# Optimization experiments

Measured on AMD Instinct MI355X. Metric: run time of the kernel, lower is better.

The kernel has to match this reference:

```python
import jax, jax.numpy as jnp
import numpy as np

NODE_SIZE = 50000
REL_SIZE = 2000
TRIPLE_SIZE = 1000000
HID = 128
DEPTH = 2


def _rows_covering(key, n_rows, n_seg):
    # sorted row indices guaranteeing every segment appears at least once
    extra = jax.random.randint(key, (n_rows - n_seg,), 0, n_seg)
    return jnp.sort(jnp.concatenate([jnp.arange(n_seg), extra])).astype(jnp.int32)


def setup_inputs() -> dict:
    key = jax.random.key(0)
    ks = jax.random.split(key, 12)
    adj = jnp.stack([_rows_covering(ks[0], TRIPLE_SIZE, NODE_SIZE),
                     jax.random.randint(ks[1], (TRIPLE_SIZE,), 0, NODE_SIZE, dtype=jnp.int32)])
    r_index = jnp.stack([jnp.arange(TRIPLE_SIZE, dtype=jnp.int32),
                         jax.random.randint(ks[2], (TRIPLE_SIZE,), 0, REL_SIZE, dtype=jnp.int32)])
    r_val = jax.random.uniform(ks[3], (TRIPLE_SIZE,), dtype=jnp.float32)
    ent_adj = jnp.stack([_rows_covering(ks[4], TRIPLE_SIZE, NODE_SIZE),
                         jax.random.randint(ks[5], (TRIPLE_SIZE,), 0, NODE_SIZE, dtype=jnp.int32)])
    rel_adj = jnp.stack([_rows_covering(ks[6], TRIPLE_SIZE, NODE_SIZE),
                         jax.random.randint(ks[7], (TRIPLE_SIZE,), 0, REL_SIZE, dtype=jnp.int32)])
    ent_emb = jax.random.normal(ks[8], (NODE_SIZE, HID), dtype=jnp.float32) * 0.05
    rel_emb = jax.random.normal(ks[9], (REL_SIZE, HID), dtype=jnp.float32) * 0.05
    attn_e = jax.random.normal(ks[10], (DEPTH, HID, 1), dtype=jnp.float32) * 0.1
    attn_r = jax.random.normal(ks[11], (DEPTH, HID, 1), dtype=jnp.float32) * 0.1
    return {"ent_emb": ent_emb, "rel_emb": rel_emb, "attn_e": attn_e, "attn_r": attn_r,
            "adj": adj, "r_index": r_index, "r_val": r_val,
            "ent_adj": ent_adj, "rel_adj": rel_adj}


def _avg(adj, emb, node_size):
    # sparse softmax over all-ones values == mean over neighbors
    rows, cols = adj[0], adj[1]
    deg = jax.ops.segment_sum(jnp.ones_like(rows, dtype=emb.dtype), rows, node_size)
    s = jax.ops.segment_sum(emb[cols], rows, node_size)  # [node_size, d]
    return s / jnp.maximum(deg, 1.0)[:, None]


def _segment_softmax(vals, seg, num_seg):
    m = jax.ops.segment_max(vals, seg, num_seg)
    e = jnp.exp(vals - m[seg])
    s = jax.ops.segment_sum(e, seg, num_seg)
    return e / s[seg]


def _nr_graph_attention(features, rel_emb, adj, r_index, r_val, attn_kernels):
    feats = jnp.tanh(features)
    outs = [feats]
    src, dst = adj[0], adj[1]
    for l in range(DEPTH):
        # sparse [T, R] @ rel_emb -> per-triple relation vector
        tri_rel = jax.ops.segment_sum(r_val[:, None] * rel_emb[r_index[1]], r_index[0], TRIPLE_SIZE)
        tri_rel = tri_rel / jnp.maximum(jnp.linalg.norm(tri_rel, axis=1, keepdims=True), 1e-12)
        neighs = feats[dst]  # [T, H]
        # Householder reflection of neighbor feature about tri_rel
        neighs = neighs - 2.0 * jnp.sum(neighs * tri_rel, axis=1, keepdims=True) * tri_rel
        att = jnp.squeeze(tri_rel @ attn_kernels[l], axis=-1)  # [T]
        a = _segment_softmax(att, src, NODE_SIZE)
        feats = jnp.tanh(jax.ops.segment_sum(neighs * a[:, None], src, NODE_SIZE))
        outs.append(feats)
    return jnp.concatenate(outs, axis=-1)  # [N, H*(DEPTH+1)]


def reference(ent_emb, rel_emb, attn_e, attn_r, adj, r_index, r_val, ent_adj, rel_adj):
    ent_feature = _avg(ent_adj, ent_emb, NODE_SIZE)  # [N, H]
    rel_feature = _avg(rel_adj, rel_emb, NODE_SIZE)  # [N, H]
    out_rel = _nr_graph_attention(rel_feature, rel_emb, adj, r_index, r_val, attn_r)
    out_ent = _nr_graph_attention(ent_feature, rel_emb, adj, r_index, r_val, attn_e)
    return jnp.concatenate([out_ent, out_rel], axis=-1)  # dropout rate 0 -> identity
```

## Files before the change

kernel.cpp:

```cpp
#include <hip/hip_runtime.h>
#include <hip/hip_fp16.h>
#include <math.h>

#define NN 50000
#define NR 2000
#define NT 1000000
#define HID 128
#define OSTRIDE 768
#define CH 256

typedef float f32x4 __attribute__((ext_vector_type(4)));
typedef unsigned u32x4 __attribute__((ext_vector_type(4)));
typedef unsigned u32x2 __attribute__((ext_vector_type(2)));
typedef _Float16 h16x2 __attribute__((ext_vector_type(2)));
typedef _Float16 h16x8 __attribute__((ext_vector_type(8)));

union U4H8 { u32x4 u; h16x8 h; };

__device__ __forceinline__ float wsum64(float v) {
#pragma unroll
  for (int off = 32; off > 0; off >>= 1) v += __shfl_xor(v, off, 64);
  return v;
}
__device__ __forceinline__ unsigned pack2(float x, float y) {
  __half2 h = __floats2half2_rn(x, y);
  union { __half2 h; unsigned u; } c; c.h = h; return c.u;
}
__device__ __forceinline__ float2 unpack2(unsigned u) {
  union { unsigned u; __half2 h; } c; c.u = u;
  return __half22float2(c.h);
}
__device__ __forceinline__ void nt_store4(const float4& v, float* p) {
  f32x4 t = {v.x, v.y, v.z, v.w};
  __builtin_nontemporal_store(t, (f32x4*)p);
}

__global__ void rowptr3_kernel(const int* __restrict__ a0, int* __restrict__ r0,
                               const int* __restrict__ a1, int* __restrict__ r1,
                               const int* __restrict__ a2, int* __restrict__ r2) {
  const int* rows = (blockIdx.y == 0) ? a0 : (blockIdx.y == 1) ? a1 : a2;
  int* rp = (blockIdx.y == 0) ? r0 : (blockIdx.y == 1) ? r1 : r2;
  int i = blockIdx.x * blockDim.x + threadIdx.x;
  int stride = gridDim.x * blockDim.x;
  for (int t = i; t < NT; t += stride) {
    if (t == 0 || rows[t] != rows[t - 1]) rp[rows[t]] = t;
  }
  if (i == 0) rp[NN] = NT;
}

__global__ __launch_bounds__(256) void prep_kernel(
    const float* __restrict__ rel_emb, const float* __restrict__ attn_e,
    const float* __restrict__ attn_r, float4* __restrict__ e4,
    float* __restrict__ n2i_arr, const float* __restrict__ ent_emb,
    __half* __restrict__ enth, __half* __restrict__ relh) {
  int wid = (blockIdx.x * blockDim.x + threadIdx.x) >> 6;
  int lane = threadIdx.x & 63;
  if (wid < NR) {
    const float2* e2 = (const float2*)rel_emb;
    float2 e = e2[(size_t)wid * 64 + lane];
    float p = wsum64(e.x * e.x + e.y * e.y);
    float inv_n = rsqrtf(p);
    const float* ks[4] = {attn_e, attn_e + HID, attn_r, attn_r + HID};
    float d[4];
#pragma unroll
    for (int j = 0; j < 4; ++j) {
      float2 a = ((const float2*)ks[j])[lane];
      d[j] = wsum64(e.x * a.x + e.y * a.y);
    }
    if (lane == 0) {
      e4[wid] = make_float4(expf(d[0] * inv_n), expf(d[1] * inv_n),
                            expf(d[2] * inv_n), expf(d[3] * inv_n));
      n2i_arr[wid] = 1.f / p;
    }
    return;
  }
  int i = (wid - NR) * 64 + lane;
  const int entu = NN * 16;
  const float4* s4;
  u32x4* d;
  int j;
  if (i < entu) {
    s4 = (const float4*)ent_emb; d = (u32x4*)enth; j = i;
  } else {
    j = i - entu;
    if (j >= NR * 16) return;
    s4 = (const float4*)rel_emb; d = (u32x4*)relh;
  }
  float4 a = s4[2 * j], b = s4[2 * j + 1];
  u32x4 w;
  w.x = pack2(a.x, a.y); w.y = pack2(a.z, a.w);
  w.z = pack2(b.x, b.y); w.w = pack2(b.z, b.w);
  __builtin_nontemporal_store(w, d + j);
}

__global__ __launch_bounds__(256) void avgwpre_kernel(
    const int* __restrict__ rp_ent, const int* __restrict__ cols_ent,
    const int* __restrict__ rp_rel, const int* __restrict__ cols_rel,
    const __half* __restrict__ enth, const __half* __restrict__ relh,
    float* __restrict__ out, __half* __restrict__ c0h,
    const int* __restrict__ rp_adj, const int* __restrict__ dst,
    const int* __restrict__ rel_id, const float* __restrict__ r_val,
    const float4* __restrict__ e4, const float* __restrict__ n2i_arr,
    unsigned* __restrict__ pk, u32x2* __restrict__ wq0,
    u32x2* __restrict__ wq1) {
  int wid = (blockIdx.x * blockDim.x + threadIdx.x) >> 6;
  int lane = threadIdx.x & 63;

  if (wid < NN) {
    int br = (wid >= NN / 2) ? 1 : 0;
    int pair = wid - br * (NN / 2);
    int node = pair * 2 + (lane >> 5);
    int sl = lane & 31;
    const int* rp = br ? rp_rel : rp_ent;
    const int* cols = br ? cols_rel : cols_ent;
    const u32x2* eb = (const u32x2*)(br ? relh : enth);
    int t0 = rp[node], t1 = rp[node + 1];
    int nmax = t1 - 1;
    int i0 = cols[t0];
    int i1 = cols[min(t0 + 1, nmax)];
    int i2 = cols[min(t0 + 2, nmax)];
    int i3 = cols[min(t0 + 3, nmax)];
    int i4 = cols[min(t0 + 4, nmax)];
    int i5 = cols[min(t0 + 5, nmax)];
    int i6 = cols[min(t0 + 6, nmax)];
    int i7 = cols[min(t0 + 7, nmax)];
    float4 acc = make_float4(0.f, 0.f, 0.f, 0.f);
    const u32x2 z = {0u, 0u};
    for (int t = t0; t < t1; t += 8) {
      u32x2 h0 = eb[(size_t)i0 * 32 + sl];
      u32x2 h1 = eb[(size_t)i1 * 32 + sl];
      u32x2 h2 = eb[(size_t)i2 * 32 + sl];
      u32x2 h3 = eb[(size_t)i3 * 32 + sl];
      u32x2 h4 = eb[(size_t)i4 * 32 + sl];
      u32x2 h5 = eb[(size_t)i5 * 32 + sl];
      u32x2 h6 = eb[(size_t)i6 * 32 + sl];
      u32x2 h7 = eb[(size_t)i7 * 32 + sl];
      int tn = t + 8;
      i0 = cols[min(tn, nmax)];
      i1 = cols[min(tn + 1, nmax)];
      i2 = cols[min(tn + 2, nmax)];
      i3 = cols[min(tn + 3, nmax)];
      i4 = cols[min(tn + 4, nmax)];
      i5 = cols[min(tn + 5, nmax)];
      i6 = cols[min(tn + 6, nmax)];
      i7 = cols[min(tn + 7, nmax)];
      h1 = (t + 1 < t1) ? h1 : z;
      h2 = (t + 2 < t1) ? h2 : z;
      h3 = (t + 3 < t1) ? h3 : z;
      h4 = (t + 4 < t1) ? h4 : z;
      h5 = (t + 5 < t1) ? h5 : z;
      h6 = (t + 6 < t1) ? h6 : z;
      h7 = (t + 7 < t1) ? h7 : z;
      float2 a0 = unpack2(h0.x), b0 = unpack2(h0.y);
      float2 a1 = unpack2(h1.x), b1 = unpack2(h1.y);
      float2 a2 = unpack2(h2.x), b2 = unpack2(h2.y);
      float2 a3 = unpack2(h3.x), b3 = unpack2(h3.y);
      float2 a4 = unpack2(h4.x), b4 = unpack2(h4.y);
      float2 a5 = unpack2(h5.x), b5 = unpack2(h5.y);
      float2 a6 = unpack2(h6.x), b6 = unpack2(h6.y);
      float2 a7 = unpack2(h7.x), b7 = unpack2(h7.y);
      acc.x += ((a0.x + a1.x) + (a2.x + a3.x)) + ((a4.x + a5.x) + (a6.x + a7.x));
      acc.y += ((a0.y + a1.y) + (a2.y + a3.y)) + ((a4.y + a5.y) + (a6.y + a7.y));
      acc.z += ((b0.x + b1.x) + (b2.x + b3.x)) + ((b4.x + b5.x) + (b6.x + b7.x));
      acc.w += ((b0.y + b1.y) + (b2.y + b3.y)) + ((b4.y + b5.y) + (b6.y + b7.y));
    }
    float inv = 1.f / (float)(t1 - t0);
    float4 o;
    o.x = tanhf(acc.x * inv); o.y = tanhf(acc.y * inv);
    o.z = tanhf(acc.z * inv); o.w = tanhf(acc.w * inv);
    nt_store4(o, out + (size_t)node * OSTRIDE + (br ? 3 * HID : 0) + sl * 4);
    u32x2 w; w.x = pack2(o.x, o.y); w.y = pack2(o.z, o.w);
    __builtin_nontemporal_store(w,
        (u32x2*)(c0h + (size_t)node * CH + br * HID + sl * 4));
    return;
  }

  wid -= NN;
  if (wid >= NN / 4) return;
  int sub = lane >> 4;
  int s = lane & 15;
  int node = wid * 4 + sub;
  int t0 = rp_adj[node], t1 = rp_adj[node + 1];
  float4 ss = make_float4(0.f, 0.f, 0.f, 0.f);
  for (int t = t0 + s; t < t1; t += 16) {
    int r = rel_id[t];
    float rv = r_val[t];
    float4 ex = e4[r];
    if (rv <= 0.f) ex = make_float4(1.f, 1.f, 1.f, 1.f);
    ss.x += ex.x; ss.y += ex.y; ss.z += ex.z; ss.w += ex.w;
  }
#pragma unroll
  for (int off = 1; off < 16; off <<= 1) {
    ss.x += __shfl_xor(ss.x, off, 64);
    ss.y += __shfl_xor(ss.y, off, 64);
    ss.z += __shfl_xor(ss.z, off, 64);
    ss.w += __shfl_xor(ss.w, off, 64);
  }
  float4 inv = make_float4(1.f / ss.x, 1.f / ss.y, 1.f / ss.z, 1.f / ss.w);
  for (int t = t0 + s; t < t1; t += 16) {
    int r = rel_id[t];
    float rv = r_val[t];
    int dn = dst[t];
    float4 ex = e4[r];
    float zi = n2i_arr[r];
    if (rv <= 0.f) { ex = make_float4(1.f, 1.f, 1.f, 1.f); zi = 0.f; }
    float we0 = ex.x * inv.x, wr0 = ex.z * inv.z;
    float we1 = ex.y * inv.y, wr1 = ex.w * inv.w;
    __builtin_nontemporal_store((unsigned)dn | ((unsigned)r << 16), pk + t);
    u32x2 a, b;
    a.x = pack2(we0, wr0); a.y = pack2(-2.f * we0 * zi, -2.f * wr0 * zi);
    b.x = pack2(we1, wr1); b.y = pack2(-2.f * we1 * zi, -2.f * wr1 * zi);
    __builtin_nontemporal_store(a, wq0 + t);
    __builtin_nontemporal_store(b, wq1 + t);
  }
}

struct RecT { int dn; int r; float we, wr, ce, cr; };

__device__ __forceinline__ RecT ldrec(int t, int t1,
                                      const unsigned* __restrict__ pk,
                                      const u32x2* __restrict__ wq) {
  bool valid = (t < t1);
  int tc = valid ? t : (t1 - 1);
  unsigned p = pk[tc];
  u32x2 w = wq[tc];
  RecT rec;
  rec.dn = (int)(p & 0xFFFFu);
  rec.r = (int)(p >> 16);
  float2 a = unpack2(w.x);
  float2 b = unpack2(w.y);
  rec.we = valid ? a.x : 0.f;
  rec.wr = valid ? a.y : 0.f;
  rec.ce = valid ? b.x : 0.f;
  rec.cr = valid ? b.y : 0.f;
  return rec;
}

__global__ __launch_bounds__(256) void attn_kernel(
    float* __restrict__ out, const int* __restrict__ rp,
    const unsigned* __restrict__ pk, const u32x2* __restrict__ wq,
    const __half* __restrict__ relh, const __half* __restrict__ chin,
    __half* __restrict__ chout, int layer) {
  int wid = (blockIdx.x * blockDim.x + threadIdx.x) >> 6;
  int lane = threadIdx.x & 63;
  if (wid >= NN) return;
  int g = lane >> 4;
  int sl = lane & 15;
  int t0 = rp[wid], t1 = rp[wid + 1];

  const u32x4* relh4 = (const u32x4*)relh;
  RecT A = ldrec(t0 + g, t1, pk, wq);
  RecT B = ldrec(t0 + 4 + g, t1, pk, wq);
  float aE[8], aR[8];
#pragma unroll
  for (int i = 0; i < 8; ++i) { aE[i] = 0.f; aR[i] = 0.f; }

  for (int tb = t0; tb < t1; tb += 8) {
    U4H8 uhA, ehA, qhA, uhB, ehB, qhB;
    uhA.u = relh4[(size_t)A.r * 16 + sl];
    const u32x4* phA = (const u32x4*)chin + (size_t)A.dn * 32;
    ehA.u = phA[sl];
    qhA.u = phA[16 + sl];
    uhB.u = relh4[(size_t)B.r * 16 + sl];
    const u32x4* phB = (const u32x4*)chin + (size_t)B.dn * 32;
    ehB.u = phB[sl];
    qhB.u = phB[16 + sl];
    RecT An = ldrec(tb + 8 + g, t1, pk, wq);
    RecT Bn = ldrec(tb + 12 + g, t1, pk, wq);

    float deA = 0.f, drA = 0.f, deB = 0.f, drB = 0.f;
#if __has_builtin(__builtin_amdgcn_fdot2)
#pragma unroll
    for (int i = 0; i < 4; ++i) {
      h16x2 uA = {uhA.h[2 * i], uhA.h[2 * i + 1]};
      h16x2 eA = {ehA.h[2 * i], ehA.h[2 * i + 1]};
      h16x2 qA = {qhA.h[2 * i], qhA.h[2 * i + 1]};
      h16x2 uB = {uhB.h[2 * i], uhB.h[2 * i + 1]};
      h16x2 eB = {ehB.h[2 * i], ehB.h[2 * i + 1]};
      h16x2 qB = {qhB.h[2 * i], qhB.h[2 * i + 1]};
      deA = __builtin_amdgcn_fdot2(uA, eA, deA, false);
      drA = __builtin_amdgcn_fdot2(uA, qA, drA, false);
      deB = __builtin_amdgcn_fdot2(uB, eB, deB, false);
      drB = __builtin_amdgcn_fdot2(uB, qB, drB, false);
    }
#else
#pragma unroll
    for (int i = 0; i < 8; ++i) {
      deA += (float)uhA.h[i] * (float)ehA.h[i];
      drA += (float)uhA.h[i] * (float)qhA.h[i];
      deB += (float)uhB.h[i] * (float)ehB.h[i];
      drB += (float)uhB.h[i] * (float)qhB.h[i];
    }
#endif
#pragma unroll
    for (int off = 1; off < 16; off <<= 1) {
      deA += __shfl_xor(deA, off, 64);
      drA += __shfl_xor(drA, off, 64);
      deB += __shfl_xor(deB, off, 64);
      drB += __shfl_xor(drB, off, 64);
    }
    float ceA = A.ce * deA;
    float crA = A.cr * drA;
    float ceB = B.ce * deB;
    float crB = B.cr * drB;
#pragma unroll
    for (int i = 0; i < 8; ++i) {
      float ufA = (float)uhA.h[i];
      float ufB = (float)uhB.h[i];
      aE[i] += A.we * (float)ehA.h[i] + ceA * ufA;
      aE[i] += B.we * (float)ehB.h[i] + ceB * ufB;
      aR[i] += A.wr * (float)qhA.h[i] + crA * ufA;
      aR[i] += B.wr * (float)qhB.h[i] + crB * ufB;
    }
    A = An;
    B = Bn;
  }

#pragma unroll
  for (int i = 0; i < 8; ++i) {
    aE[i] += __shfl_xor(aE[i], 16, 64);
    aE[i] += __shfl_xor(aE[i], 32, 64);
    aR[i] += __shfl_xor(aR[i], 16, 64);
    aR[i] += __shfl_xor(aR[i], 32, 64);
  }

  float4 v;
  if (g == 0) v = make_float4(aE[0], aE[1], aE[2], aE[3]);
  else if (g == 1) v = make_float4(aE[4], aE[5], aE[6], aE[7]);
  else if (g == 2) v = make_float4(aR[0], aR[1], aR[2], aR[3]);
  else v = make_float4(aR[4], aR[5], aR[6], aR[7]);
  v.x = tanhf(v.x); v.y = tanhf(v.y); v.z = tanhf(v.z); v.w = tanhf(v.w);
  float* ob = (g < 2) ? (out + (size_t)wid * OSTRIDE + (layer + 1) * HID)
                      : (out + (size_t)wid * OSTRIDE + (4 + layer) * HID);
  nt_store4(v, ob + sl * 8 + (g & 1) * 4);
  if (chout) {
    u32x2 w; w.x = pack2(v.x, v.y); w.y = pack2(v.z, v.w);
    __builtin_nontemporal_store(
        w, (u32x2*)(chout + (size_t)wid * CH + (g >> 1) * 128 + sl * 8 + (g & 1) * 4));
  }
}

extern "C" void kernel_launch(void* const* d_in, const int* in_sizes, int n_in,
                              void* d_out, int out_size, void* d_ws, size_t ws_size,
                              hipStream_t stream) {
  const float* ent_emb = (const float*)d_in[0];
  const float* rel_emb = (const float*)d_in[1];
  const float* attn_e = (const float*)d_in[2];
  const float* attn_r = (const float*)d_in[3];
  const int* adj = (const int*)d_in[4];
  const int* r_index = (const int*)d_in[5];
  const float* r_val = (const float*)d_in[6];
  const int* ent_adj = (const int*)d_in[7];
  const int* rel_adj = (const int*)d_in[8];
  float* out = (float*)d_out;

  char* ws = (char*)d_ws;
  __half* enth = (__half*)ws;  ws += (size_t)NN * HID * sizeof(__half);
  __half* relh = (__half*)ws;  ws += (size_t)NR * HID * sizeof(__half);
  __half* C0h = (__half*)ws;   ws += (size_t)NN * CH * sizeof(__half);
  __half* C1h = (__half*)ws;   ws += (size_t)NN * CH * sizeof(__half);
  unsigned* pk = (unsigned*)ws; ws += (size_t)NT * sizeof(unsigned);
  u32x2* wq0 = (u32x2*)ws;     ws += (size_t)NT * sizeof(u32x2);
  u32x2* wq1 = (u32x2*)ws;     ws += (size_t)NT * sizeof(u32x2);
  float4* e4 = (float4*)ws;    ws += (size_t)NR * sizeof(float4);
  float* n2i = (float*)ws;     ws += (size_t)NR * sizeof(float);
  int* rp_adj = (int*)ws;      ws += (NN + 1) * sizeof(int);
  int* rp_ent = (int*)ws;      ws += (NN + 1) * sizeof(int);
  int* rp_rel = (int*)ws;      ws += (NN + 1) * sizeof(int);

  dim3 rg(512, 3);
  rowptr3_kernel<<<rg, 256, 0, stream>>>(adj, rp_adj, ent_adj, rp_ent, rel_adj, rp_rel);
  prep_kernel<<<3750, 256, 0, stream>>>(rel_emb, attn_e, attn_r, e4, n2i,
                                        ent_emb, enth, relh);
  avgwpre_kernel<<<15625, 256, 0, stream>>>(
      rp_ent, ent_adj + NT, rp_rel, rel_adj + NT, enth, relh, out, C0h,
      rp_adj, adj + NT, r_index + NT, r_val, e4, n2i, pk, wq0, wq1);
  for (int l = 0; l < 2; ++l) {
    attn_kernel<<<(NN * 64) / 256, 256, 0, stream>>>(
        out, rp_adj, pk, (l == 0) ? wq0 : wq1, relh,
        (l == 0) ? C0h : C1h, (l == 0) ? C1h : nullptr, l);
  }
}
```

Baseline: 467.7 us.

## Fuse rowptr into prep, prenormalize relation rows, shrink per-edge weight records

Merges the row-pointer construction into the prep kernel, removing one launch. Adds a half-precision table of unit-normalized relation embeddings, with a zero row for invalid relations, so the per-edge Householder coefficient is computed as -2*w*dot instead of being stored. This halves the per-edge weight records from 8 to 4 bytes. It also reduces the attention loop from two to one edge batch per iteration, which lowers register pressure but gives less memory-level parallelism per wave.

After: 439.5 us. -6.0%, faster.

```diff
diff --git a/kernel.cpp b/kernel.cpp
--- a/kernel.cpp
+++ b/kernel.cpp
@@ -9,6 +9,12 @@
 #define OSTRIDE 768
 #define CH 256
 
+#define PREP_CVT_W (NR + 1)
+#define PREP_CVT_NW 13000
+#define PREP_RP_W (PREP_CVT_W + PREP_CVT_NW)
+#define PREP_RP_NW 46875
+#define PREP_TOT_W (PREP_RP_W + PREP_RP_NW)
+
 typedef float f32x4 __attribute__((ext_vector_type(4)));
 typedef unsigned u32x4 __attribute__((ext_vector_type(4)));
 typedef unsigned u32x2 __attribute__((ext_vector_type(2)));
@@ -35,31 +41,23 @@
   __builtin_nontemporal_store(t, (f32x4*)p);
 }
 
-__global__ void rowptr3_kernel(const int* __restrict__ a0, int* __restrict__ r0,
-                               const int* __restrict__ a1, int* __restrict__ r1,
-                               const int* __restrict__ a2, int* __restrict__ r2) {
-  const int* rows = (blockIdx.y == 0) ? a0 : (blockIdx.y == 1) ? a1 : a2;
-  int* rp = (blockIdx.y == 0) ? r0 : (blockIdx.y == 1) ? r1 : r2;
-  int i = blockIdx.x * blockDim.x + threadIdx.x;
-  int stride = gridDim.x * blockDim.x;
-  for (int t = i; t < NT; t += stride) {
-    if (t == 0 || rows[t] != rows[t - 1]) rp[rows[t]] = t;
-  }
-  if (i == 0) rp[NN] = NT;
-}
-
 __global__ __launch_bounds__(256) void prep_kernel(
     const float* __restrict__ rel_emb, const float* __restrict__ attn_e,
-    const float* __restrict__ attn_r, float4* __restrict__ e4,
-    float* __restrict__ n2i_arr, const float* __restrict__ ent_emb,
-    __half* __restrict__ enth, __half* __restrict__ relh) {
+    const float* __restrict__ attn_r, const float* __restrict__ ent_emb,
+    float4* __restrict__ e4, __half* __restrict__ enth,
+    __half* __restrict__ relh, __half* __restrict__ relnh,
+    const int* __restrict__ rows_adj, const int* __restrict__ rows_ent,
+    const int* __restrict__ rows_rel, int* __restrict__ rp_adj,
+    int* __restrict__ rp_ent, int* __restrict__ rp_rel) {
   int wid = (blockIdx.x * blockDim.x + threadIdx.x) >> 6;
   int lane = threadIdx.x & 63;
+
   if (wid < NR) {
     const float2* e2 = (const float2*)rel_emb;
     float2 e = e2[(size_t)wid * 64 + lane];
     float p = wsum64(e.x * e.x + e.y * e.y);
     float inv_n = rsqrtf(p);
+    ((unsigned*)relnh)[(size_t)wid * 64 + lane] = pack2(e.x * inv_n, e.y * inv_n);
     const float* ks[4] = {attn_e, attn_e + HID, attn_r, attn_r + HID};
     float d[4];
 #pragma unroll
@@ -70,27 +68,42 @@
     if (lane == 0) {
       e4[wid] = make_float4(expf(d[0] * inv_n), expf(d[1] * inv_n),
                             expf(d[2] * inv_n), expf(d[3] * inv_n));
-      n2i_arr[wid] = 1.f / p;
     }
     return;
   }
-  int i = (wid - NR) * 64 + lane;
-  const int entu = NN * 16;
-  const float4* s4;
-  u32x4* d;
-  int j;
-  if (i < entu) {
-    s4 = (const float4*)ent_emb; d = (u32x4*)enth; j = i;
-  } else {
-    j = i - entu;
-    if (j >= NR * 16) return;
-    s4 = (const float4*)rel_emb; d = (u32x4*)relh;
-  }
-  float4 a = s4[2 * j], b = s4[2 * j + 1];
-  u32x4 w;
-  w.x = pack2(a.x, a.y); w.y = pack2(a.z, a.w);
-  w.z = pack2(b.x, b.y); w.w = pack2(b.z, b.w);
-  __builtin_nontemporal_store(w, d + j);
+  if (wid == NR) {
+    ((unsigned*)relnh)[(size_t)NR * 64 + lane] = 0u;
+    if (lane == 0) { rp_adj[NN] = NT; rp_ent[NN] = NT; rp_rel[NN] = NT; }
+    return;
+  }
+  if (wid < PREP_RP_W) {
+    int i = (wid - PREP_CVT_W) * 64 + lane;
+    const int entu = NN * 16;
+    const float4* s4;
+    u32x4* d;
+    int j;
+    if (i < entu) {
+      s4 = (const float4*)ent_emb; d = (u32x4*)enth; j = i;
+    } else {
+      j = i - entu;
+      if (j >= NR * 16) return;
+      s4 = (const float4*)rel_emb; d = (u32x4*)relh;
+    }
+    float4 a = s4[2 * j], b = s4[2 * j + 1];
+    u32x4 w;
+    w.x = pack2(a.x, a.y); w.y = pack2(a.z, a.w);
+    w.z = pack2(b.x, b.y); w.w = pack2(b.z, b.w);
+    __builtin_nontemporal_store(w, d + j);
+    return;
+  }
+  if (wid >= PREP_TOT_W) return;
+  int idx = (wid - PREP_RP_W) * 64 + lane;
+  int arr = idx / NT;
+  int t = idx - arr * NT;
+  const int* rows = (arr == 0) ? rows_adj : (arr == 1) ? rows_ent : rows_rel;
+  int* rp = (arr == 0) ? rp_adj : (arr == 1) ? rp_ent : rp_rel;
+  int rcur = rows[t];
+  if (t == 0 || rows[t - 1] != rcur) rp[rcur] = t;
 }
 
 __global__ __launch_bounds__(256) void avgwpre_kernel(
@@ -100,9 +113,8 @@
     float* __restrict__ out, __half* __restrict__ c0h,
     const int* __restrict__ rp_adj, const int* __restrict__ dst,
     const int* __restrict__ rel_id, const float* __restrict__ r_val,
-    const float4* __restrict__ e4, const float* __restrict__ n2i_arr,
-    unsigned* __restrict__ pk, u32x2* __restrict__ wq0,
-    u32x2* __restrict__ wq1) {
+    const float4* __restrict__ e4, unsigned* __restrict__ pk,
+    unsigned* __restrict__ wq0, unsigned* __restrict__ wq1) {
   int wid = (blockIdx.x * blockDim.x + threadIdx.x) >> 6;
   int lane = threadIdx.x & 63;
 
@@ -202,44 +214,40 @@
     float rv = r_val[t];
     int dn = dst[t];
     float4 ex = e4[r];
-    float zi = n2i_arr[r];
-    if (rv <= 0.f) { ex = make_float4(1.f, 1.f, 1.f, 1.f); zi = 0.f; }
+    int ru = r;
+    if (rv <= 0.f) {
+      ex = make_float4(1.f, 1.f, 1.f, 1.f);
+      ru = NR;
+    }
     float we0 = ex.x * inv.x, wr0 = ex.z * inv.z;
     float we1 = ex.y * inv.y, wr1 = ex.w * inv.w;
-    __builtin_nontemporal_store((unsigned)dn | ((unsigned)r << 16), pk + t);
-    u32x2 a, b;
-    a.x = pack2(we0, wr0); a.y = pack2(-2.f * we0 * zi, -2.f * wr0 * zi);
-    b.x = pack2(we1, wr1); b.y = pack2(-2.f * we1 * zi, -2.f * wr1 * zi);
-    __builtin_nontemporal_store(a, wq0 + t);
-    __builtin_nontemporal_store(b, wq1 + t);
-  }
-}
-
-struct RecT { int dn; int r; float we, wr, ce, cr; };
+    __builtin_nontemporal_store((unsigned)dn | ((unsigned)ru << 16), pk + t);
+    __builtin_nontemporal_store(pack2(we0, wr0), wq0 + t);
+    __builtin_nontemporal_store(pack2(we1, wr1), wq1 + t);
+  }
+}
+
+struct RecT { int dn; int r; float we, wr; };
 
 __device__ __forceinline__ RecT ldrec(int t, int t1,
                                       const unsigned* __restrict__ pk,
-                                      const u32x2* __restrict__ wq) {
+                                      const unsigned* __restrict__ wq) {
   bool valid = (t < t1);
   int tc = valid ? t : (t1 - 1);
   unsigned p = pk[tc];
-  u32x2 w = wq[tc];
+  float2 a = unpack2(wq[tc]);
   RecT rec;
   rec.dn = (int)(p & 0xFFFFu);
   rec.r = (int)(p >> 16);
-  float2 a = unpack2(w.x);
-  float2 b = unpack2(w.y);
   rec.we = valid ? a.x : 0.f;
   rec.wr = valid ? a.y : 0.f;
-  rec.ce = valid ? b.x : 0.f;
-  rec.cr = valid ? b.y : 0.f;
   return rec;
 }
 
 __global__ __launch_bounds__(256) void attn_kernel(
     float* __restrict__ out, const int* __restrict__ rp,
-    const unsigned* __restrict__ pk, const u32x2* __restrict__ wq,
-    const __half* __restrict__ relh, const __half* __restrict__ chin,
+    const unsigned* __restrict__ pk, const unsigned* __restrict__ wq,
+    const __half* __restrict__ relnh, const __half* __restrict__ chin,
     __half* __restrict__ chout, int layer) {
   int wid = (blockIdx.x * blockDim.x + threadIdx.x) >> 6;
   int lane = threadIdx.x & 63;
@@ -248,72 +256,51 @@
   int sl = lane & 15;
   int t0 = rp[wid], t1 = rp[wid + 1];
 
-  const u32x4* relh4 = (const u32x4*)relh;
-  RecT A = ldrec(t0 + g, t1, pk, wq);
-  RecT B = ldrec(t0 + 4 + g, t1, pk, wq);
+  const u32x4* relnh4 = (const u32x4*)relnh;
+  RecT b0 = ldrec(t0 + g, t1, pk, wq);
   float aE[8], aR[8];
 #pragma unroll
   for (int i = 0; i < 8; ++i) { aE[i] = 0.f; aR[i] = 0.f; }
 
-  for (int tb = t0; tb < t1; tb += 8) {
-    U4H8 uhA, ehA, qhA, uhB, ehB, qhB;
-    uhA.u = relh4[(size_t)A.r * 16 + sl];
-    const u32x4* phA = (const u32x4*)chin + (size_t)A.dn * 32;
-    ehA.u = phA[sl];
-    qhA.u = phA[16 + sl];
-    uhB.u = relh4[(size_t)B.r * 16 + sl];
-    const u32x4* phB = (const u32x4*)chin + (size_t)B.dn * 32;
-    ehB.u = phB[sl];
-    qhB.u = phB[16 + sl];
-    RecT An = ldrec(tb + 8 + g, t1, pk, wq);
-    RecT Bn = ldrec(tb + 12 + g, t1, pk, wq);
-
-    float deA = 0.f, drA = 0.f, deB = 0.f, drB = 0.f;
+  for (int tb = t0; tb < t1; tb += 4) {
+    U4H8 uh, eh, qh;
+    uh.u = relnh4[(size_t)b0.r * 16 + sl];
+    const u32x4* ph = (const u32x4*)chin + (size_t)b0.dn * 32;
+    eh.u = ph[sl];
+    qh.u = ph[16 + sl];
+    RecT b1 = ldrec(tb + 4 + g, t1, pk, wq);
+
+    float de = 0.f, dr = 0.f;
 #if __has_builtin(__builtin_amdgcn_fdot2)
 #pragma unroll
     for (int i = 0; i < 4; ++i) {
-      h16x2 uA = {uhA.h[2 * i], uhA.h[2 * i + 1]};
-      h16x2 eA = {ehA.h[2 * i], ehA.h[2 * i + 1]};
-      h16x2 qA = {qhA.h[2 * i], qhA.h[2 * i + 1]};
-      h16x2 uB = {uhB.h[2 * i], uhB.h[2 * i + 1]};
-      h16x2 eB = {ehB.h[2 * i], ehB.h[2 * i + 1]};
-      h16x2 qB = {qhB.h[2 * i], qhB.h[2 * i + 1]};
-      deA = __builtin_amdgcn_fdot2(uA, eA, deA, false);
-      drA = __builtin_amdgcn_fdot2(uA, qA, drA, false);
-      deB = __builtin_amdgcn_fdot2(uB, eB, deB, false);
-      drB = __builtin_amdgcn_fdot2(uB, qB, drB, false);
+      h16x2 up = {uh.h[2 * i], uh.h[2 * i + 1]};
+      h16x2 ep = {eh.h[2 * i], eh.h[2 * i + 1]};
+      h16x2 qp = {qh.h[2 * i], qh.h[2 * i + 1]};
+      de = __builtin_amdgcn_fdot2(up, ep, de, false);
+      dr = __builtin_amdgcn_fdot2(up, qp, dr, false);
     }
 #else
 #pragma unroll
     for (int i = 0; i < 8; ++i) {
-      deA += (float)uhA.h[i] * (float)ehA.h[i];
-      drA += (float)uhA.h[i] * (float)qhA.h[i];
-      deB += (float)uhB.h[i] * (float)ehB.h[i];
-      drB += (float)uhB.h[i] * (float)qhB.h[i];
+      de += (float)uh.h[i] * (float)eh.h[i];
+      dr += (float)uh.h[i] * (float)qh.h[i];
     }
 #endif
 #pragma unroll
     for (int off = 1; off < 16; off <<= 1) {
-      deA += __shfl_xor(deA, off, 64);
-      drA += __shfl_xor(drA, off, 64);
-      deB += __shfl_xor(deB, off, 64);
-      drB += __shfl_xor(drB, off, 64);
-    }
-    float ceA = A.ce * deA;
-    float crA = A.cr * drA;
-    float ceB = B.ce * deB;
-    float crB = B.cr * drB;
+      de += __shfl_xor(de, off, 64);
+      dr += __shfl_xor(dr, off, 64);
+    }
+    float ce = -2.f * b0.we * de;
+    float cr = -2.f * b0.wr * dr;
 #pragma unroll
     for (int i = 0; i < 8; ++i) {
-      float ufA = (float)uhA.h[i];
-      float ufB = (float)uhB.h[i];
-      aE[i] += A.we * (float)ehA.h[i] + ceA * ufA;
-      aE[i] += B.we * (float)ehB.h[i] + ceB * ufB;
-      aR[i] += A.wr * (float)qhA.h[i] + crA * ufA;
-      aR[i] += B.wr * (float)qhB.h[i] + crB * ufB;
-    }
-    A = An;
-    B = Bn;
+      float uf = (float)uh.h[i];
+      aE[i] += b0.we * (float)eh.h[i] + ce * uf;
+      aR[i] += b0.wr * (float)qh.h[i] + cr * uf;
+    }
+    b0 = b1;
   }
 
 #pragma unroll
@@ -355,29 +342,28 @@
   float* out = (float*)d_out;
 
   char* ws = (char*)d_ws;
-  __half* enth = (__half*)ws;  ws += (size_t)NN * HID * sizeof(__half);
-  __half* relh = (__half*)ws;  ws += (size_t)NR * HID * sizeof(__half);
-  __half* C0h = (__half*)ws;   ws += (size_t)NN * CH * sizeof(__half);
-  __half* C1h = (__half*)ws;   ws += (size_t)NN * CH * sizeof(__half);
-  unsigned* pk = (unsigned*)ws; ws += (size_t)NT * sizeof(unsigned);
-  u32x2* wq0 = (u32x2*)ws;     ws += (size_t)NT * sizeof(u32x2);
-  u32x2* wq1 = (u32x2*)ws;     ws += (size_t)NT * sizeof(u32x2);
-  float4* e4 = (float4*)ws;    ws += (size_t)NR * sizeof(float4);
-  float* n2i = (float*)ws;     ws += (size_t)NR * sizeof(float);
-  int* rp_adj = (int*)ws;      ws += (NN + 1) * sizeof(int);
-  int* rp_ent = (int*)ws;      ws += (NN + 1) * sizeof(int);
-  int* rp_rel = (int*)ws;      ws += (NN + 1) * sizeof(int);
-
-  dim3 rg(512, 3);
-  rowptr3_kernel<<<rg, 256, 0, stream>>>(adj, rp_adj, ent_adj, rp_ent, rel_adj, rp_rel);
-  prep_kernel<<<3750, 256, 0, stream>>>(rel_emb, attn_e, attn_r, e4, n2i,
-                                        ent_emb, enth, relh);
+  __half* enth = (__half*)ws;   ws += (size_t)NN * HID * sizeof(__half);
+  __half* relh = (__half*)ws;   ws += (size_t)NR * HID * sizeof(__half);
+  __half* relnh = (__half*)ws;  ws += (size_t)(NR + 1) * HID * sizeof(__half);
+  __half* C0h = (__half*)ws;    ws += (size_t)NN * CH * sizeof(__half);
+  __half* C1h = (__half*)ws;    ws += (size_t)NN * CH * sizeof(__half);
+  unsigned* pk = (unsigned*)ws;  ws += (size_t)NT * sizeof(unsigned);
+  unsigned* wq0 = (unsigned*)ws; ws += (size_t)NT * sizeof(unsigned);
+  unsigned* wq1 = (unsigned*)ws; ws += (size_t)NT * sizeof(unsigned);
+  float4* e4 = (float4*)ws;     ws += (size_t)NR * sizeof(float4);
+  int* rp_adj = (int*)ws;       ws += (NN + 1) * sizeof(int);
+  int* rp_ent = (int*)ws;       ws += (NN + 1) * sizeof(int);
+  int* rp_rel = (int*)ws;       ws += (NN + 1) * sizeof(int);
+
+  prep_kernel<<<(PREP_TOT_W + 3) / 4, 256, 0, stream>>>(
+      rel_emb, attn_e, attn_r, ent_emb, e4, enth, relh, relnh,
+      adj, ent_adj, rel_adj, rp_adj, rp_ent, rp_rel);
   avgwpre_kernel<<<15625, 256, 0, stream>>>(
       rp_ent, ent_adj + NT, rp_rel, rel_adj + NT, enth, relh, out, C0h,
-      rp_adj, adj + NT, r_index + NT, r_val, e4, n2i, pk, wq0, wq1);
+      rp_adj, adj + NT, r_index + NT, r_val, e4, pk, wq0, wq1);
   for (int l = 0; l < 2; ++l) {
     attn_kernel<<<(NN * 64) / 256, 256, 0, stream>>>(
-        out, rp_adj, pk, (l == 0) ? wq0 : wq1, relh,
+        out, rp_adj, pk, (l == 0) ? wq0 : wq1, relnh,
         (l == 0) ? C0h : C1h, (l == 0) ? C1h : nullptr, l);
   }
 }
```
